# Kernel tuning notes

Measured on AMD Instinct MI355X. Metric: run time of the kernel, lower is better.

## Reference

```python
import jax, jax.numpy as jnp
import numpy as np

B, T, DIN, DOUT = 32, 128, 1024, 1024


def _linear_params(key, din, dout):
    # matches torch nn.Linear default init: U(-1/sqrt(din), 1/sqrt(din))
    kw, kb = jax.random.split(key)
    s = 1.0 / np.sqrt(din)
    W = jax.random.uniform(kw, (dout, din), minval=-s, maxval=s, dtype=jnp.float32)
    b = jax.random.uniform(kb, (dout,), minval=-s, maxval=s, dtype=jnp.float32)
    return W, b


def setup_inputs() -> dict:
    key = jax.random.key(0)
    kx, kz1, kz2, kr1, kr2, kh1, kh2 = jax.random.split(key, 7)
    x = jax.random.normal(kx, (B, T, DIN), dtype=jnp.float32)
    Wz, bz = _linear_params(kz1, DIN, DOUT)   # w_z
    Uz, cz = _linear_params(kz2, DOUT, DOUT)  # u_z
    Wr, br = _linear_params(kr1, DIN, DOUT)   # w_r
    Ur, cr = _linear_params(kr2, DOUT, DOUT)  # u_r
    Wh, bh = _linear_params(kh1, DIN, DOUT)   # w_h
    Uh, ch = _linear_params(kh2, DOUT, DOUT)  # u_h
    return {"x": x, "Wz": Wz, "bz": bz, "Uz": Uz, "cz": cz,
            "Wr": Wr, "br": br, "Ur": Ur, "cr": cr,
            "Wh": Wh, "bh": bh, "Uh": Uh, "ch": ch}


def reference(x, Wz, bz, Uz, cz, Wr, br, Ur, cr, Wh, bh, Uh, ch):
    # manyToManyGRU with simultaneous=True, bias=False, both activations sigmoid.
    # b_z/b_r/b_h are zero buffers (bias=False) and thus omitted.
    batch, seq, _ = x.shape
    dout = Wz.shape[0]
    h0 = jnp.zeros((batch, dout), dtype=x.dtype)

    def step(h, xt):
        z = jax.nn.sigmoid(xt @ Wz.T + bz + h @ Uz.T + cz)
        r = jax.nn.sigmoid(xt @ Wr.T + br + h @ Ur.T + cr)
        h_hat = jax.nn.sigmoid(xt @ Wh.T + bh + (r * h) @ Uh.T + ch)
        h_new = (1.0 - z) * h + z * h_hat
        return h_new, h_new

    _, ys = jax.lax.scan(step, h0, jnp.swapaxes(x, 0, 1))  # ys: (T, B, D)
    # Original torch code cats per-step (B,D) outputs on dim 0 -> (T*B, D)
    # then reshapes to (B, T, D); reproduce that exact memory reinterpretation.
    return ys.reshape(batch, seq, dout)
```

## Files before the change

### kernel.cpp

```cpp
#include <hip/hip_runtime.h>
#include <stdint.h>

typedef unsigned short u16;
typedef unsigned long long u64;
typedef __attribute__((ext_vector_type(8))) short short8;
typedef __attribute__((ext_vector_type(4))) float f32x4;

#define CNT_OFF    0
#define FLG_OFF    131072
#define BS_OFF     135168
#define H64_OFF    147456
#define ZERO_BYTES (H64_OFF + 262144)
#define RH64_OFF   ZERO_BYTES
#define XB_OFF     (1<<20)
#define WB_OFF     (9<<20)
#define WS_FULL    (21u<<20)
#define REP_STRIDE 8192

__device__ __forceinline__ float bf2f(u16 v) {
    unsigned u = ((unsigned)v) << 16;
    return __builtin_bit_cast(float, u);
}
__device__ __forceinline__ u16 f2bf(float f) {
    unsigned u = __builtin_bit_cast(unsigned, f);
    unsigned r = 0x7fffu + ((u >> 16) & 1u);
    return (u16)((u + r) >> 16);
}
__device__ __forceinline__ float sigm(float x) { return 1.0f / (1.0f + __expf(-x)); }

__device__ __forceinline__ short8 cvt8f(const float* f) {
    short8 r;
#pragma unroll
    for (int j = 0; j < 8; j++) r[j] = (short)f2bf(f[j]);
    return r;
}
__device__ __forceinline__ short8 cvt8any(const void* src, long ei, unsigned isbf) {
    if (isbf) return *(const short8*)((const u16*)src + ei);
    return cvt8f((const float*)src + ei);
}

union Q2 { u64 q[2]; short8 s; };
__device__ __forceinline__ short8 ld_coh8(const u64* p) {
    Q2 u;
    u.q[0] = __hip_atomic_load(p,     __ATOMIC_RELAXED, __HIP_MEMORY_SCOPE_AGENT);
    u.q[1] = __hip_atomic_load(p + 1, __ATOMIC_RELAXED, __HIP_MEMORY_SCOPE_AGENT);
    return u.s;
}
__device__ __forceinline__ u64 ld64(const u64* p) {
    return __hip_atomic_load(p, __ATOMIC_RELAXED, __HIP_MEMORY_SCOPE_AGENT);
}
__device__ __forceinline__ unsigned ld_flag(const unsigned* p) {
    return __hip_atomic_load(p, __ATOMIC_RELAXED, __HIP_MEMORY_SCOPE_AGENT);
}
__device__ __forceinline__ void st_flag(unsigned* p, unsigned v) {
    __hip_atomic_store(p, v, __ATOMIC_RELAXED, __HIP_MEMORY_SCOPE_AGENT);
}
__device__ __forceinline__ void st64(u64* p, u64 v) {
    __hip_atomic_store(p, v, __ATOMIC_RELAXED, __HIP_MEMORY_SCOPE_AGENT);
}

__device__ __forceinline__ void gbar(unsigned* flgs, unsigned e, unsigned nb) {
    __syncthreads();
    const unsigned tid = threadIdx.x;
    if (tid < 4)
        st_flag(flgs + blockIdx.x * 256 + tid * 64, e);
    if (tid < nb) {
        const unsigned* fp = flgs + tid * 256 + (blockIdx.x & 3) * 64;
        while (ld_flag(fp) < e)
            __builtin_amdgcn_s_sleep(1);
    }
    __syncthreads();
}

struct Ptrs { const void* p[13]; };

__global__ __launch_bounds__(256) void detect_k(Ptrs ps, unsigned* flags) {
    const u16* a = (const u16*)ps.p[blockIdx.x];
    __shared__ int tot;
    if (threadIdx.x == 0) tot = 0;
    __syncthreads();
    int cnt = 0;
    for (int i = threadIdx.x; i < 1024; i += 256) {
        unsigned u = a[i];
        unsigned e = (u >> 7) & 0xFF;
        cnt += (e == 0 || (e >= 100 && e <= 140)) ? 1 : 0;
    }
    atomicAdd(&tot, cnt);
    __syncthreads();
    if (threadIdx.x == 0) flags[blockIdx.x] = (tot >= 920) ? 1u : 0u;
}

struct SPtrs { const void* x; const void* W[6]; const void* b[6]; };

__global__ __launch_bounds__(256) void stage_k(SPtrs ps, const unsigned* __restrict__ flags,
                                               u16* __restrict__ xb, u16* __restrict__ wb,
                                               float* __restrict__ bs, int do_x) {
    int blk = blockIdx.x, tid = threadIdx.x;
    int xblocks = do_x ? 2048 : 0;
    if (blk < xblocks) {
        long ei = ((long)blk * 256 + tid) * 8;
        *(short8*)(xb + ei) = cvt8any(ps.x, ei, flags[0]);
    } else if (blk < xblocks + 6 * 512) {
        int r = (blk - xblocks) >> 9;
        const int fidx[6] = {1, 3, 5, 7, 9, 11};
        long ei = ((long)((blk - xblocks) & 511) * 256 + tid) * 8;
        *(short8*)(wb + (long)r * 1048576 + ei) = cvt8any(ps.W[r], ei, flags[fidx[r]]);
    } else {
        const int fb[3] = {2, 6, 10}, fc[3] = {4, 8, 12};
        for (int g = 0; g < 3; g++)
            for (int i = tid; i < 1024; i += 256) {
                float b = flags[fb[g]] ? bf2f(((const u16*)ps.b[2 * g])[i])
                                       : ((const float*)ps.b[2 * g])[i];
                float c = flags[fc[g]] ? bf2f(((const u16*)ps.b[2 * g + 1])[i])
                                       : ((const float*)ps.b[2 * g + 1])[i];
                bs[g * 1024 + i] = b + c;
            }
    }
}

__global__ __launch_bounds__(1024, 4) void gru_rec(
    const void* __restrict__ xbase, int xmode,
    const u16* __restrict__ wb, const float* __restrict__ bs,
    u64* __restrict__ h64, u64* __restrict__ rh64,
    const unsigned* __restrict__ flags,
    unsigned* __restrict__ flgs,
    void* __restrict__ out)
{
    const int tid  = threadIdx.x;
    const int lane = tid & 63, wave = tid >> 6;
    const int quad = lane >> 4, ln = lane & 15;
    const int blk  = blockIdx.x;
    const unsigned NB = gridDim.x;
    const int rep  = blk & 3;

    const unsigned xisbf = xmode ? 1u : flags[0];
    const unsigned outbf = flags[0];

    const int ct = blk >> 1, rt = blk & 1;
    const int R = rt * 16, C0 = ct * 16;

    const int gA  = wave >> 2, kqA = wave & 3;
    const int kb0 = kqA * 256;
    const int wmapA[4] = {3, 2, 1, 0};
    const u16* BwA = wb + (long)wmapA[gA] * 1048576 + (C0 + ln) * 1024 + kb0 + quad * 8;
    const bool hA  = (gA == 0) || (gA == 2);
    const int hsc  = (kb0 >> 2) + quad * 2;
    const long xAo = ((long)(R + ln) * 128) * 1024 + kb0 + quad * 8;

    const int gB  = wave >> 3, keB = wave & 7;
    const int kb1 = keB * 128;
    const u16* BwB = wb + (long)(gB ? 4 : 5) * 1048576 + (C0 + ln) * 1024 + kb1 + quad * 8;
    const u64* rhq = rh64 + rep * REP_STRIDE + (R + ln) * 256 + (kb1 >> 2) + quad * 2;
    const long xBo = ((long)(R + ln) * 128) * 1024 + kb1 + quad * 8;

    const float bias_z = bs[C0 + ln];
    const float bias_r = bs[1024 + C0 + ln];
    const float bias_h = bs[2048 + C0 + ln];

    __shared__ float sA[16][4][64];
    __shared__ float zt[4][64];
    __shared__ float ht[4][64];
    __shared__ u16   tT[16][20];
    __shared__ u64   hs[16][258];

    if (wave == 0)
#pragma unroll
        for (int r = 0; r < 4; r++) ht[r][lane] = 0.f;
    __syncthreads();

    const int prow = lane >> 2, pseg = lane & 3;

    const u64* hsrc = h64 + rep * REP_STRIDE + (R + wave) * 256 + lane;

    for (int t = 0; t < 128; t++) {
        {
#pragma unroll
            for (int c = 0; c < 4; c++)
                hs[wave][lane + 64 * c] = ld64(hsrc + 64 * c);
        }
        __syncthreads();
        {
            f32x4 acc = (f32x4){0.f, 0.f, 0.f, 0.f};
            const long xo = xAo + (long)t * 1024;
#pragma unroll
            for (int i = 0; i < 8; i++) {
                short8 a = hA ? *(const short8*)&hs[ln][hsc + i * 8]
                              : cvt8any(xbase, xo + i * 32, xisbf);
                acc = __builtin_amdgcn_mfma_f32_16x16x32_bf16(
                    a, *(const short8*)(BwA + i * 32), acc, 0, 0, 0);
            }
#pragma unroll
            for (int r = 0; r < 4; r++) sA[wave][r][lane] = acc[r];
        }
        __syncthreads();
        if (wave == 0) {
#pragma unroll
            for (int r = 0; r < 4; r++) {
                float s = bias_r;
#pragma unroll
                for (int w = 0; w < 8; w++) s += sA[w][r][lane];
                float rv = sigm(s);
                tT[quad * 4 + r][ln] = f2bf(rv * ht[r][lane]);
            }
            u64 v = (u64)tT[prow][pseg * 4] | ((u64)tT[prow][pseg * 4 + 1] << 16)
                  | ((u64)tT[prow][pseg * 4 + 2] << 32) | ((u64)tT[prow][pseg * 4 + 3] << 48);
            u64* dst = &rh64[(R + prow) * 256 + ct * 4 + pseg];
#pragma unroll
            for (int rp = 0; rp < 4; rp++) st64(dst + rp * REP_STRIDE, v);
        } else if (wave == 1) {
#pragma unroll
            for (int r = 0; r < 4; r++) {
                float s = bias_z;
#pragma unroll
                for (int w = 8; w < 16; w++) s += sA[w][r][lane];
                zt[r][lane] = sigm(s);
            }
        }
        gbar(flgs, 2 * t + 1, NB);
        {
            f32x4 acc = (f32x4){0.f, 0.f, 0.f, 0.f};
            const long xo = xBo + (long)t * 1024;
#pragma unroll
            for (int i = 0; i < 4; i++) {
                short8 a = (gB == 0) ? ld_coh8(rhq + i * 8)
                                     : cvt8any(xbase, xo + i * 32, xisbf);
                acc = __builtin_amdgcn_mfma_f32_16x16x32_bf16(
                    a, *(const short8*)(BwB + i * 32), acc, 0, 0, 0);
            }
#pragma unroll
            for (int r = 0; r < 4; r++) sA[wave][r][lane] = acc[r];
        }
        __syncthreads();
        if (wave == 0) {
#pragma unroll
            for (int r = 0; r < 4; r++) {
                float s = bias_h;
#pragma unroll
                for (int w = 0; w < 16; w++) s += sA[w][r][lane];
                float hh = sigm(s);
                float z  = zt[r][lane];
                float hv = ht[r][lane];
                float hn = (1.0f - z) * hv + z * hh;
                ht[r][lane] = hn;
                u16 hb = f2bf(hn);
                int row = quad * 4 + r;
                tT[row][ln] = hb;
                long oi = ((long)(t * 32) + R + row) * 1024 + C0 + ln;
                if (outbf) ((u16*)out)[oi] = hb;
                else       ((float*)out)[oi] = hn;
            }
            u64 v = (u64)tT[prow][pseg * 4] | ((u64)tT[prow][pseg * 4 + 1] << 16)
                  | ((u64)tT[prow][pseg * 4 + 2] << 32) | ((u64)tT[prow][pseg * 4 + 3] << 48);
            u64* dst = &h64[(R + prow) * 256 + ct * 4 + pseg];
#pragma unroll
            for (int rp = 0; rp < 4; rp++) st64(dst + rp * REP_STRIDE, v);
        }
        if (t < 127) gbar(flgs, 2 * t + 2, NB);
    }
}

extern "C" void kernel_launch(void* const* d_in, const int* in_sizes, int n_in,
                              void* d_out, int out_size, void* d_ws, size_t ws_size,
                              hipStream_t stream)
{
    char* ws = (char*)d_ws;
    hipMemsetAsync(d_ws, 0, ZERO_BYTES, stream);

    unsigned* flgs  = (unsigned*)(ws + CNT_OFF);
    unsigned* flags = (unsigned*)(ws + FLG_OFF);
    float*    bs    = (float*)(ws + BS_OFF);
    u64*      h64   = (u64*)(ws + H64_OFF);
    u64*      rh64  = (u64*)(ws + RH64_OFF);
    u16*      xb    = (u16*)(ws + XB_OFF);

    Ptrs dp;
    for (int i = 0; i < 13; i++) dp.p[i] = d_in[i];
    detect_k<<<13, 256, 0, stream>>>(dp, flags);

    SPtrs sp;
    sp.x = d_in[0];
    sp.W[0] = d_in[1];  sp.W[1] = d_in[3];
    sp.W[2] = d_in[5];  sp.W[3] = d_in[7];
    sp.W[4] = d_in[9];  sp.W[5] = d_in[11];
    sp.b[0] = d_in[2];  sp.b[1] = d_in[4];
    sp.b[2] = d_in[6];  sp.b[3] = d_in[8];
    sp.b[4] = d_in[10]; sp.b[5] = d_in[12];

    if (ws_size >= WS_FULL) {
        u16* wbuf = (u16*)(ws + WB_OFF);
        stage_k<<<2048 + 6 * 512 + 1, 256, 0, stream>>>(sp, flags, xb, wbuf, bs, 1);
        gru_rec<<<128, 1024, 0, stream>>>(xb, 1, wbuf, bs, h64, rh64, flags, flgs, d_out);
    } else {
        u16* wbuf = (u16*)(ws + XB_OFF);
        stage_k<<<6 * 512 + 1, 256, 0, stream>>>(sp, flags, xb, wbuf, bs, 0);
        gru_rec<<<128, 1024, 0, stream>>>(d_in[0], 0, wbuf, bs, h64, rh64, flags, flgs, d_out);
    }
}
```

Before: 1.430 ms.

## Double columns per block and halve the grid of the recurrent GRU kernel

```diff
diff --git a/kernel.cpp b/kernel.cpp
--- a/kernel.cpp
+++ b/kernel.cpp
@@ -137,7 +137,7 @@
     const unsigned outbf = flags[0];
 
     const int ct = blk >> 1, rt = blk & 1;
-    const int R = rt * 16, C0 = ct * 16;
+    const int R = rt * 16, C0 = ct * 32;
 
     const int gA  = wave >> 2, kqA = wave & 3;
     const int kb0 = kqA * 256;
@@ -153,19 +153,23 @@
     const u64* rhq = rh64 + rep * REP_STRIDE + (R + ln) * 256 + (kb1 >> 2) + quad * 2;
     const long xBo = ((long)(R + ln) * 128) * 1024 + kb1 + quad * 8;
 
-    const float bias_z = bs[C0 + ln];
-    const float bias_r = bs[1024 + C0 + ln];
-    const float bias_h = bs[2048 + C0 + ln];
-
-    __shared__ float sA[16][4][64];
-    __shared__ float zt[4][64];
-    __shared__ float ht[4][64];
-    __shared__ u16   tT[16][20];
+    float bias_z[2], bias_r[2], bias_h[2];
+#pragma unroll
+    for (int s = 0; s < 2; s++) {
+        bias_z[s] = bs[C0 + s * 16 + ln];
+        bias_r[s] = bs[1024 + C0 + s * 16 + ln];
+        bias_h[s] = bs[2048 + C0 + s * 16 + ln];
+    }
+
+    __shared__ float sA[16][2][4][64];
+    __shared__ float zt[2][4][64];
+    __shared__ float ht[2][4][64];
+    __shared__ u16   tT[2][16][20];
     __shared__ u64   hs[16][258];
 
-    if (wave == 0)
-#pragma unroll
-        for (int r = 0; r < 4; r++) ht[r][lane] = 0.f;
+    if (wave < 2)
+#pragma unroll
+        for (int r = 0; r < 4; r++) ht[wave][r][lane] = 0.f;
     __syncthreads();
 
     const int prow = lane >> 2, pseg = lane & 3;
@@ -180,78 +184,93 @@
         }
         __syncthreads();
         {
-            f32x4 acc = (f32x4){0.f, 0.f, 0.f, 0.f};
+            f32x4 a0 = (f32x4){0.f, 0.f, 0.f, 0.f};
+            f32x4 a1 = (f32x4){0.f, 0.f, 0.f, 0.f};
             const long xo = xAo + (long)t * 1024;
 #pragma unroll
             for (int i = 0; i < 8; i++) {
                 short8 a = hA ? *(const short8*)&hs[ln][hsc + i * 8]
                               : cvt8any(xbase, xo + i * 32, xisbf);
-                acc = __builtin_amdgcn_mfma_f32_16x16x32_bf16(
-                    a, *(const short8*)(BwA + i * 32), acc, 0, 0, 0);
-            }
-#pragma unroll
-            for (int r = 0; r < 4; r++) sA[wave][r][lane] = acc[r];
+                a0 = __builtin_amdgcn_mfma_f32_16x16x32_bf16(
+                    a, *(const short8*)(BwA + i * 32), a0, 0, 0, 0);
+                a1 = __builtin_amdgcn_mfma_f32_16x16x32_bf16(
+                    a, *(const short8*)(BwA + 16384 + i * 32), a1, 0, 0, 0);
+            }
+#pragma unroll
+            for (int r = 0; r < 4; r++) {
+                sA[wave][0][r][lane] = a0[r];
+                sA[wave][1][r][lane] = a1[r];
+            }
         }
         __syncthreads();
-        if (wave == 0) {
-#pragma unroll
-            for (int r = 0; r < 4; r++) {
-                float s = bias_r;
-#pragma unroll
-                for (int w = 0; w < 8; w++) s += sA[w][r][lane];
-                float rv = sigm(s);
-                tT[quad * 4 + r][ln] = f2bf(rv * ht[r][lane]);
-            }
-            u64 v = (u64)tT[prow][pseg * 4] | ((u64)tT[prow][pseg * 4 + 1] << 16)
-                  | ((u64)tT[prow][pseg * 4 + 2] << 32) | ((u64)tT[prow][pseg * 4 + 3] << 48);
-            u64* dst = &rh64[(R + prow) * 256 + ct * 4 + pseg];
+        if (wave < 2) {
+            const int s = wave;
+#pragma unroll
+            for (int r = 0; r < 4; r++) {
+                float v = bias_r[s];
+#pragma unroll
+                for (int w = 0; w < 8; w++) v += sA[w][s][r][lane];
+                float rv = sigm(v);
+                tT[s][quad * 4 + r][ln] = f2bf(rv * ht[s][r][lane]);
+            }
+            u64 v = (u64)tT[s][prow][pseg * 4] | ((u64)tT[s][prow][pseg * 4 + 1] << 16)
+                  | ((u64)tT[s][prow][pseg * 4 + 2] << 32) | ((u64)tT[s][prow][pseg * 4 + 3] << 48);
+            u64* dst = &rh64[(R + prow) * 256 + ct * 8 + s * 4 + pseg];
 #pragma unroll
             for (int rp = 0; rp < 4; rp++) st64(dst + rp * REP_STRIDE, v);
-        } else if (wave == 1) {
-#pragma unroll
-            for (int r = 0; r < 4; r++) {
-                float s = bias_z;
-#pragma unroll
-                for (int w = 8; w < 16; w++) s += sA[w][r][lane];
-                zt[r][lane] = sigm(s);
+        } else if (wave < 4) {
+            const int s = wave - 2;
+#pragma unroll
+            for (int r = 0; r < 4; r++) {
+                float v = bias_z[s];
+#pragma unroll
+                for (int w = 8; w < 16; w++) v += sA[w][s][r][lane];
+                zt[s][r][lane] = sigm(v);
             }
         }
         gbar(flgs, 2 * t + 1, NB);
         {
-            f32x4 acc = (f32x4){0.f, 0.f, 0.f, 0.f};
+            f32x4 b0 = (f32x4){0.f, 0.f, 0.f, 0.f};
+            f32x4 b1 = (f32x4){0.f, 0.f, 0.f, 0.f};
             const long xo = xBo + (long)t * 1024;
 #pragma unroll
             for (int i = 0; i < 4; i++) {
                 short8 a = (gB == 0) ? ld_coh8(rhq + i * 8)
                                      : cvt8any(xbase, xo + i * 32, xisbf);
-                acc = __builtin_amdgcn_mfma_f32_16x16x32_bf16(
-                    a, *(const short8*)(BwB + i * 32), acc, 0, 0, 0);
-            }
-#pragma unroll
-            for (int r = 0; r < 4; r++) sA[wave][r][lane] = acc[r];
+                b0 = __builtin_amdgcn_mfma_f32_16x16x32_bf16(
+                    a, *(const short8*)(BwB + i * 32), b0, 0, 0, 0);
+                b1 = __builtin_amdgcn_mfma_f32_16x16x32_bf16(
+                    a, *(const short8*)(BwB + 16384 + i * 32), b1, 0, 0, 0);
+            }
+#pragma unroll
+            for (int r = 0; r < 4; r++) {
+                sA[wave][0][r][lane] = b0[r];
+                sA[wave][1][r][lane] = b1[r];
+            }
         }
         __syncthreads();
-        if (wave == 0) {
-#pragma unroll
-            for (int r = 0; r < 4; r++) {
-                float s = bias_h;
-#pragma unroll
-                for (int w = 0; w < 16; w++) s += sA[w][r][lane];
-                float hh = sigm(s);
-                float z  = zt[r][lane];
-                float hv = ht[r][lane];
+        if (wave < 2) {
+            const int s = wave;
+#pragma unroll
+            for (int r = 0; r < 4; r++) {
+                float v = bias_h[s];
+#pragma unroll
+                for (int w = 0; w < 16; w++) v += sA[w][s][r][lane];
+                float hh = sigm(v);
+                float z  = zt[s][r][lane];
+                float hv = ht[s][r][lane];
                 float hn = (1.0f - z) * hv + z * hh;
-                ht[r][lane] = hn;
+                ht[s][r][lane] = hn;
                 u16 hb = f2bf(hn);
                 int row = quad * 4 + r;
-                tT[row][ln] = hb;
-                long oi = ((long)(t * 32) + R + row) * 1024 + C0 + ln;
+                tT[s][row][ln] = hb;
+                long oi = ((long)(t * 32) + R + row) * 1024 + C0 + s * 16 + ln;
                 if (outbf) ((u16*)out)[oi] = hb;
                 else       ((float*)out)[oi] = hn;
             }
-            u64 v = (u64)tT[prow][pseg * 4] | ((u64)tT[prow][pseg * 4 + 1] << 16)
-                  | ((u64)tT[prow][pseg * 4 + 2] << 32) | ((u64)tT[prow][pseg * 4 + 3] << 48);
-            u64* dst = &h64[(R + prow) * 256 + ct * 4 + pseg];
+            u64 v = (u64)tT[s][prow][pseg * 4] | ((u64)tT[s][prow][pseg * 4 + 1] << 16)
+                  | ((u64)tT[s][prow][pseg * 4 + 2] << 32) | ((u64)tT[s][prow][pseg * 4 + 3] << 48);
+            u64* dst = &h64[(R + prow) * 256 + ct * 8 + s * 4 + pseg];
 #pragma unroll
             for (int rp = 0; rp < 4; rp++) st64(dst + rp * REP_STRIDE, v);
         }
@@ -289,10 +308,10 @@
     if (ws_size >= WS_FULL) {
         u16* wbuf = (u16*)(ws + WB_OFF);
         stage_k<<<2048 + 6 * 512 + 1, 256, 0, stream>>>(sp, flags, xb, wbuf, bs, 1);
-        gru_rec<<<128, 1024, 0, stream>>>(xb, 1, wbuf, bs, h64, rh64, flags, flgs, d_out);
+        gru_rec<<<64, 1024, 0, stream>>>(xb, 1, wbuf, bs, h64, rh64, flags, flgs, d_out);
     } else {
         u16* wbuf = (u16*)(ws + XB_OFF);
         stage_k<<<6 * 512 + 1, 256, 0, stream>>>(sp, flags, xb, wbuf, bs, 0);
-        gru_rec<<<128, 1024, 0, stream>>>(d_in[0], 0, wbuf, bs, h64, rh64, flags, flgs, d_out);
-    }
-}
+        gru_rec<<<64, 1024, 0, stream>>>(d_in[0], 0, wbuf, bs, h64, rh64, flags, flgs, d_out);
+    }
+}
```

Measured after the change: 2.077 ms. +45.2%, slower.

## Split grid barrier per row-tile and use wide coherent loads for hidden state

Applied to the files above, without the earlier changes.

```diff
diff --git a/kernel.cpp b/kernel.cpp
--- a/kernel.cpp
+++ b/kernel.cpp
@@ -5,6 +5,7 @@
 typedef unsigned long long u64;
 typedef __attribute__((ext_vector_type(8))) short short8;
 typedef __attribute__((ext_vector_type(4))) float f32x4;
+typedef __attribute__((ext_vector_type(4))) unsigned u32x4;
 
 #define CNT_OFF    0
 #define FLG_OFF    131072
@@ -39,16 +40,6 @@
     return cvt8f((const float*)src + ei);
 }
 
-union Q2 { u64 q[2]; short8 s; };
-__device__ __forceinline__ short8 ld_coh8(const u64* p) {
-    Q2 u;
-    u.q[0] = __hip_atomic_load(p,     __ATOMIC_RELAXED, __HIP_MEMORY_SCOPE_AGENT);
-    u.q[1] = __hip_atomic_load(p + 1, __ATOMIC_RELAXED, __HIP_MEMORY_SCOPE_AGENT);
-    return u.s;
-}
-__device__ __forceinline__ u64 ld64(const u64* p) {
-    return __hip_atomic_load(p, __ATOMIC_RELAXED, __HIP_MEMORY_SCOPE_AGENT);
-}
 __device__ __forceinline__ unsigned ld_flag(const unsigned* p) {
     return __hip_atomic_load(p, __ATOMIC_RELAXED, __HIP_MEMORY_SCOPE_AGENT);
 }
@@ -59,13 +50,36 @@
     __hip_atomic_store(p, v, __ATOMIC_RELAXED, __HIP_MEMORY_SCOPE_AGENT);
 }
 
-__device__ __forceinline__ void gbar(unsigned* flgs, unsigned e, unsigned nb) {
+__device__ __forceinline__ void ld2_coh16(u32x4* d0, u32x4* d1,
+                                          const u64* p0, const u64* p1) {
+    asm volatile(
+        "global_load_dwordx4 %0, %2, off sc0 sc1\n\t"
+        "global_load_dwordx4 %1, %3, off sc0 sc1\n\t"
+        "s_waitcnt vmcnt(0)"
+        : "=&v"(*d0), "=&v"(*d1)
+        : "v"(p0), "v"(p1)
+        : "memory");
+}
+__device__ __forceinline__ void ld4_coh16(u32x4* d0, u32x4* d1, u32x4* d2, u32x4* d3,
+                                          const u64* p) {
+    asm volatile(
+        "global_load_dwordx4 %0, %4, off sc0 sc1\n\t"
+        "global_load_dwordx4 %1, %5, off sc0 sc1\n\t"
+        "global_load_dwordx4 %2, %6, off sc0 sc1\n\t"
+        "global_load_dwordx4 %3, %7, off sc0 sc1\n\t"
+        "s_waitcnt vmcnt(0)"
+        : "=&v"(*d0), "=&v"(*d1), "=&v"(*d2), "=&v"(*d3)
+        : "v"(p), "v"(p + 8), "v"(p + 16), "v"(p + 24)
+        : "memory");
+}
+
+__device__ __forceinline__ void gbar(unsigned* myflgs, unsigned e, int ct) {
     __syncthreads();
     const unsigned tid = threadIdx.x;
     if (tid < 4)
-        st_flag(flgs + blockIdx.x * 256 + tid * 64, e);
-    if (tid < nb) {
-        const unsigned* fp = flgs + tid * 256 + (blockIdx.x & 3) * 64;
+        st_flag(myflgs + ct * 256 + tid * 64, e);
+    if (tid < 64) {
+        const unsigned* fp = myflgs + tid * 256 + (ct & 3) * 64;
         while (ld_flag(fp) < e)
             __builtin_amdgcn_s_sleep(1);
     }
@@ -130,7 +144,6 @@
     const int lane = tid & 63, wave = tid >> 6;
     const int quad = lane >> 4, ln = lane & 15;
     const int blk  = blockIdx.x;
-    const unsigned NB = gridDim.x;
     const int rep  = blk & 3;
 
     const unsigned xisbf = xmode ? 1u : flags[0];
@@ -138,6 +151,7 @@
 
     const int ct = blk >> 1, rt = blk & 1;
     const int R = rt * 16, C0 = ct * 16;
+    unsigned* myflgs = flgs + rt * 16384;
 
     const int gA  = wave >> 2, kqA = wave & 3;
     const int kb0 = kqA * 256;
@@ -161,7 +175,7 @@
     __shared__ float zt[4][64];
     __shared__ float ht[4][64];
     __shared__ u16   tT[16][20];
-    __shared__ u64   hs[16][258];
+    __shared__ __align__(16) u64 hs[16][258];
 
     if (wave == 0)
 #pragma unroll
@@ -170,13 +184,14 @@
 
     const int prow = lane >> 2, pseg = lane & 3;
 
-    const u64* hsrc = h64 + rep * REP_STRIDE + (R + wave) * 256 + lane;
+    const u64* hsrc = h64 + rep * REP_STRIDE + (R + wave) * 256 + 2 * lane;
 
     for (int t = 0; t < 128; t++) {
         {
-#pragma unroll
-            for (int c = 0; c < 4; c++)
-                hs[wave][lane + 64 * c] = ld64(hsrc + 64 * c);
+            u32x4 d0, d1;
+            ld2_coh16(&d0, &d1, hsrc, hsrc + 128);
+            *(u32x4*)&hs[wave][2 * lane]       = d0;
+            *(u32x4*)&hs[wave][128 + 2 * lane] = d1;
         }
         __syncthreads();
         {
@@ -216,16 +231,28 @@
                 zt[r][lane] = sigm(s);
             }
         }
-        gbar(flgs, 2 * t + 1, NB);
+        gbar(myflgs, 2 * t + 1, ct);
         {
             f32x4 acc = (f32x4){0.f, 0.f, 0.f, 0.f};
-            const long xo = xBo + (long)t * 1024;
-#pragma unroll
-            for (int i = 0; i < 4; i++) {
-                short8 a = (gB == 0) ? ld_coh8(rhq + i * 8)
-                                     : cvt8any(xbase, xo + i * 32, xisbf);
-                acc = __builtin_amdgcn_mfma_f32_16x16x32_bf16(
-                    a, *(const short8*)(BwB + i * 32), acc, 0, 0, 0);
+            if (gB == 0) {
+                u32x4 m0, m1, m2, m3;
+                ld4_coh16(&m0, &m1, &m2, &m3, rhq);
+                acc = __builtin_amdgcn_mfma_f32_16x16x32_bf16(
+                    __builtin_bit_cast(short8, m0), *(const short8*)(BwB +  0), acc, 0, 0, 0);
+                acc = __builtin_amdgcn_mfma_f32_16x16x32_bf16(
+                    __builtin_bit_cast(short8, m1), *(const short8*)(BwB + 32), acc, 0, 0, 0);
+                acc = __builtin_amdgcn_mfma_f32_16x16x32_bf16(
+                    __builtin_bit_cast(short8, m2), *(const short8*)(BwB + 64), acc, 0, 0, 0);
+                acc = __builtin_amdgcn_mfma_f32_16x16x32_bf16(
+                    __builtin_bit_cast(short8, m3), *(const short8*)(BwB + 96), acc, 0, 0, 0);
+            } else {
+                const long xo = xBo + (long)t * 1024;
+#pragma unroll
+                for (int i = 0; i < 4; i++) {
+                    short8 a = cvt8any(xbase, xo + i * 32, xisbf);
+                    acc = __builtin_amdgcn_mfma_f32_16x16x32_bf16(
+                        a, *(const short8*)(BwB + i * 32), acc, 0, 0, 0);
+                }
             }
 #pragma unroll
             for (int r = 0; r < 4; r++) sA[wave][r][lane] = acc[r];
@@ -255,7 +282,7 @@
 #pragma unroll
             for (int rp = 0; rp < 4; rp++) st64(dst + rp * REP_STRIDE, v);
         }
-        if (t < 127) gbar(flgs, 2 * t + 2, NB);
+        if (t < 127) gbar(myflgs, 2 * t + 2, ct);
     }
 }
 
```

After: 1.803 ms. 1.26x slower.

## Replace grid-wide barrier with per-row-tile flag barriers and split output store

Applied to the files above, without the earlier changes.

```diff
diff --git a/kernel.cpp b/kernel.cpp
--- a/kernel.cpp
+++ b/kernel.cpp
@@ -57,19 +57,6 @@
 }
 __device__ __forceinline__ void st64(u64* p, u64 v) {
     __hip_atomic_store(p, v, __ATOMIC_RELAXED, __HIP_MEMORY_SCOPE_AGENT);
-}
-
-__device__ __forceinline__ void gbar(unsigned* flgs, unsigned e, unsigned nb) {
-    __syncthreads();
-    const unsigned tid = threadIdx.x;
-    if (tid < 4)
-        st_flag(flgs + blockIdx.x * 256 + tid * 64, e);
-    if (tid < nb) {
-        const unsigned* fp = flgs + tid * 256 + (blockIdx.x & 3) * 64;
-        while (ld_flag(fp) < e)
-            __builtin_amdgcn_s_sleep(1);
-    }
-    __syncthreads();
 }
 
 struct Ptrs { const void* p[13]; };
@@ -130,7 +117,6 @@
     const int lane = tid & 63, wave = tid >> 6;
     const int quad = lane >> 4, ln = lane & 15;
     const int blk  = blockIdx.x;
-    const unsigned NB = gridDim.x;
     const int rep  = blk & 3;
 
     const unsigned xisbf = xmode ? 1u : flags[0];
@@ -138,6 +124,7 @@
 
     const int ct = blk >> 1, rt = blk & 1;
     const int R = rt * 16, C0 = ct * 16;
+    unsigned* myflgs = flgs + rt * 16384;
 
     const int gA  = wave >> 2, kqA = wave & 3;
     const int kb0 = kqA * 256;
@@ -159,20 +146,22 @@
 
     __shared__ float sA[16][4][64];
     __shared__ float zt[4][64];
-    __shared__ float ht[4][64];
+    __shared__ float ht[2][4][64];
     __shared__ u16   tT[16][20];
-    __shared__ u64   hs[16][258];
+    __shared__ __align__(16) u64 hs[16][258];
 
     if (wave == 0)
 #pragma unroll
-        for (int r = 0; r < 4; r++) ht[r][lane] = 0.f;
+        for (int r = 0; r < 4; r++) ht[0][r][lane] = 0.f;
     __syncthreads();
 
     const int prow = lane >> 2, pseg = lane & 3;
 
     const u64* hsrc = h64 + rep * REP_STRIDE + (R + wave) * 256 + lane;
+    const unsigned* pollp = myflgs + lane * 256 + (ct & 3) * 64;
 
     for (int t = 0; t < 128; t++) {
+        const int par = t & 1;
         {
 #pragma unroll
             for (int c = 0; c < 4; c++)
@@ -200,13 +189,15 @@
 #pragma unroll
                 for (int w = 0; w < 8; w++) s += sA[w][r][lane];
                 float rv = sigm(s);
-                tT[quad * 4 + r][ln] = f2bf(rv * ht[r][lane]);
+                tT[quad * 4 + r][ln] = f2bf(rv * ht[par][r][lane]);
             }
             u64 v = (u64)tT[prow][pseg * 4] | ((u64)tT[prow][pseg * 4 + 1] << 16)
                   | ((u64)tT[prow][pseg * 4 + 2] << 32) | ((u64)tT[prow][pseg * 4 + 3] << 48);
             u64* dst = &rh64[(R + prow) * 256 + ct * 4 + pseg];
 #pragma unroll
             for (int rp = 0; rp < 4; rp++) st64(dst + rp * REP_STRIDE, v);
+            asm volatile("s_waitcnt vmcnt(0)" ::: "memory");
+            if (lane < 4) st_flag(myflgs + ct * 256 + lane * 64, 2 * t + 1);
         } else if (wave == 1) {
 #pragma unroll
             for (int r = 0; r < 4; r++) {
@@ -215,8 +206,11 @@
                 for (int w = 8; w < 16; w++) s += sA[w][r][lane];
                 zt[r][lane] = sigm(s);
             }
-        }
-        gbar(flgs, 2 * t + 1, NB);
+        } else if (wave == 15) {
+            while (ld_flag(pollp) < (unsigned)(2 * t + 1))
+                __builtin_amdgcn_s_sleep(1);
+        }
+        __syncthreads();
         {
             f32x4 acc = (f32x4){0.f, 0.f, 0.f, 0.f};
             const long xo = xBo + (long)t * 1024;
@@ -239,23 +233,39 @@
                 for (int w = 0; w < 16; w++) s += sA[w][r][lane];
                 float hh = sigm(s);
                 float z  = zt[r][lane];
-                float hv = ht[r][lane];
+                float hv = ht[par][r][lane];
                 float hn = (1.0f - z) * hv + z * hh;
-                ht[r][lane] = hn;
-                u16 hb = f2bf(hn);
-                int row = quad * 4 + r;
-                tT[row][ln] = hb;
-                long oi = ((long)(t * 32) + R + row) * 1024 + C0 + ln;
-                if (outbf) ((u16*)out)[oi] = hb;
-                else       ((float*)out)[oi] = hn;
+                ht[par ^ 1][r][lane] = hn;
+                tT[quad * 4 + r][ln] = f2bf(hn);
             }
             u64 v = (u64)tT[prow][pseg * 4] | ((u64)tT[prow][pseg * 4 + 1] << 16)
                   | ((u64)tT[prow][pseg * 4 + 2] << 32) | ((u64)tT[prow][pseg * 4 + 3] << 48);
             u64* dst = &h64[(R + prow) * 256 + ct * 4 + pseg];
 #pragma unroll
             for (int rp = 0; rp < 4; rp++) st64(dst + rp * REP_STRIDE, v);
-        }
-        if (t < 127) gbar(flgs, 2 * t + 2, NB);
+            asm volatile("s_waitcnt vmcnt(0)" ::: "memory");
+            if (lane < 4) st_flag(myflgs + ct * 256 + lane * 64, 2 * t + 2);
+        } else if (wave == 1) {
+#pragma unroll
+            for (int r = 0; r < 4; r++) {
+                float s = bias_h;
+#pragma unroll
+                for (int w = 0; w < 16; w++) s += sA[w][r][lane];
+                float hh = sigm(s);
+                float z  = zt[r][lane];
+                float hv = ht[par][r][lane];
+                float hn = (1.0f - z) * hv + z * hh;
+                int row = quad * 4 + r;
+                long oi = ((long)(t * 32) + R + row) * 1024 + C0 + ln;
+                if (outbf) ((u16*)out)[oi] = f2bf(hn);
+                else       ((float*)out)[oi] = hn;
+            }
+        } else if (wave == 15) {
+            if (t < 127)
+                while (ld_flag(pollp) < (unsigned)(2 * t + 2))
+                    __builtin_amdgcn_s_sleep(1);
+        }
+        __syncthreads();
     }
 }
 
```

After: 1.686 ms. 1.18x slower.
